# Kernel tuning notes

Measured on AMD Instinct MI355X. Metric: run time of the kernel, lower is better.

## Reference

```python
import jax, jax.numpy as jnp
import numpy as np

COST_CLASS, COST_BOX = 1.0, 5.0   # HungarianMatcher defaults
W_CLASS, W_BOX = 1.0, 5.0         # weight_dict
B, Q, M, NUM_CLASSES = 64, 900, 64, 4


def _hungarian(cost):
    """Jonker-Volgenant shortest augmenting path (same optimum as scipy's
    linear_sum_assignment). cost: [n, m] numpy, n <= m. Returns, for each
    row i, the assigned column index."""
    n, m = cost.shape
    u = np.zeros(n + 1, dtype=np.float64)
    v = np.zeros(m + 1, dtype=np.float64)
    p = np.zeros(m + 1, dtype=np.int64)    # p[j]: row matched to col j (1-based), 0=free
    way = np.zeros(m + 1, dtype=np.int64)
    cost = cost.astype(np.float64)
    for i in range(1, n + 1):
        p[0] = i
        j0 = 0
        minv = np.full(m + 1, np.inf)
        used = np.zeros(m + 1, dtype=bool)
        while True:
            used[j0] = True
            i0 = p[j0]
            cur = cost[i0 - 1, :] - u[i0] - v[1:]           # reduced costs, len m
            mask = ~used[1:]
            upd = mask & (cur < minv[1:])
            minv[1:][upd] = cur[upd]
            way[1:][upd] = j0
            cand = np.where(mask, minv[1:], np.inf)
            j1 = int(np.argmin(cand)) + 1
            delta = cand[j1 - 1]
            u[p[used]] += delta
            v[used] -= delta
            minv[1:][mask] -= delta
            j0 = j1
            if p[j0] == 0:
                break
        while j0 != 0:                                       # augment along path
            j1 = way[j0]
            p[j0] = p[j1]
            j0 = j1
    row_to_col = np.zeros(n, dtype=np.int64)
    for j in range(1, m + 1):
        if p[j] > 0:
            row_to_col[p[j] - 1] = j - 1
    return row_to_col


def _match(pred_boxes, pred_classes, gt_boxes, gt_labels, valid):
    """Host-side (no-grad) Hungarian matching, mirroring HungarianMatcher.
    Returns flat (batch_ids, pred_ids, gt_ids) numpy index arrays over all
    matched pairs; gt_ids index into the ORIGINAL [M] gt axis."""
    b_ids, p_ids, g_ids = [], [], []
    for b in range(pred_boxes.shape[0]):
        vpos = np.where(valid[b])[0]
        m = vpos.shape[0]
        if m == 0:
            continue
        logits = pred_classes[b]
        z = logits - logits.max(-1, keepdims=True)
        prob = np.exp(z)
        prob /= prob.sum(-1, keepdims=True)                  # softmax [Q, C]
        labels = gt_labels[b][vpos]
        cost_class = -prob[:, labels]                        # [Q, m]
        gb = gt_boxes[b][vpos]                               # [m, 6]
        cost_box = np.abs(pred_boxes[b][:, None, :] - gb[None, :, :]).sum(-1)  # L1 cdist [Q, m]
        cost = COST_CLASS * cost_class + COST_BOX * cost_box
        pred_idx = _hungarian(cost.T)                        # gt row -> pred col
        b_ids.append(np.full(m, b, dtype=np.int64))
        p_ids.append(pred_idx)
        g_ids.append(vpos.astype(np.int64))
    return (np.concatenate(b_ids), np.concatenate(p_ids), np.concatenate(g_ids))


def setup_inputs() -> dict:
    key = jax.random.key(0)
    k1, k2, k3, k4, k5 = jax.random.split(key, 5)
    return {
        "pred_boxes": jax.random.normal(k1, (B, Q, 6), dtype=jnp.float32),
        "pred_classes": jax.random.normal(k2, (B, Q, NUM_CLASSES), dtype=jnp.float32),
        "gt_boxes": jax.random.normal(k3, (B, M, 6), dtype=jnp.float32),
        "gt_labels": jax.random.randint(k4, (B, M), 0, NUM_CLASSES, dtype=jnp.int64),
        "gt_valid_mask": jax.random.bernoulli(k5, 0.8, (B, M)),
    }


def reference(pred_boxes, pred_classes, gt_boxes, gt_labels, gt_valid_mask):
    b_ids, p_ids, g_ids = _match(
        np.asarray(pred_boxes), np.asarray(pred_classes),
        np.asarray(gt_boxes), np.asarray(gt_labels), np.asarray(gt_valid_mask))
    n = b_ids.shape[0]
    labels = jnp.asarray(gt_labels)[b_ids, g_ids]            # [N]
    # class loss: mean cross-entropy over matched pairs
    logp = jax.nn.log_softmax(pred_classes[b_ids, p_ids], axis=-1)  # [N, C]
    class_loss = -jnp.mean(jnp.take_along_axis(logp, labels[:, None], axis=1))
    # box loss: elementwise-mean L1 over matched pairs
    box_loss = jnp.mean(jnp.abs(pred_boxes[b_ids, p_ids] - gt_boxes[b_ids, g_ids]))
    total_loss = W_CLASS * class_loss + W_BOX * box_loss
    return jnp.stack([class_loss, box_loss, total_loss])
```

## Files before the change

### kernel.cpp

```cpp
#include <hip/hip_runtime.h>
#include <cfloat>
#include <cmath>

#define NB 64
#define NQ 900
#define NM 64
#define NC 4
#define THREADS 256
#define NS 15

#define S_LIST(X) X(0) X(1) X(2) X(3) X(4) X(5) X(6) X(7) X(8) X(9) \
                  X(10) X(11) X(12) X(13) X(14)

__device__ __forceinline__ unsigned int uminu(unsigned int a, unsigned int b) {
    return a < b ? a : b;
}

__device__ __forceinline__ unsigned int wave_redmin_u32(unsigned int x) {
    int t;
    t = __builtin_amdgcn_update_dpp(-1, (int)x, 0x111, 0xF, 0xF, false);
    x = uminu(x, (unsigned)t);
    t = __builtin_amdgcn_update_dpp(-1, (int)x, 0x112, 0xF, 0xF, false);
    x = uminu(x, (unsigned)t);
    t = __builtin_amdgcn_update_dpp(-1, (int)x, 0x114, 0xF, 0xF, false);
    x = uminu(x, (unsigned)t);
    t = __builtin_amdgcn_update_dpp(-1, (int)x, 0x118, 0xF, 0xF, false);
    x = uminu(x, (unsigned)t);
    unsigned a = (unsigned)__builtin_amdgcn_readlane((int)x, 15);
    unsigned b = (unsigned)__builtin_amdgcn_readlane((int)x, 31);
    unsigned c = (unsigned)__builtin_amdgcn_readlane((int)x, 47);
    unsigned d = (unsigned)__builtin_amdgcn_readlane((int)x, 63);
    return uminu(uminu(a, b), uminu(c, d));
}

__device__ __forceinline__ void wave_argmin_f(float lmin, int lj,
                                              float& mv, int& mj) {
    unsigned u = __float_as_uint(lmin);
    unsigned key = (u & 0x80000000u) ? ~u : (u | 0x80000000u);
    unsigned mk = wave_redmin_u32(key);
    unsigned cand = (key == mk) ? (unsigned)lj : 0x7FFFFFFFu;
    mj = (int)wave_redmin_u32(cand);
    unsigned mu = (mk & 0x80000000u) ? (mk & 0x7FFFFFFFu) : ~mk;
    mv = __uint_as_float(mu);
}

__global__ __launch_bounds__(THREADS, 1) void match_kernel(
    const float* __restrict__ pred_boxes,
    const float* __restrict__ pred_classes,
    const float* __restrict__ gt_boxes,
    const unsigned int* __restrict__ labels_w,
    const unsigned int* __restrict__ mask_w,
    const unsigned char* __restrict__ mask_b,
    float* __restrict__ cls_part, float* __restrict__ box_part,
    int* __restrict__ cnt_part)
{
    __shared__ float4 pbx4[NQ];
    __shared__ float2 pbx2[NQ];
    __shared__ float  probT[NC][NQ];
    __shared__ int    pcol[NQ + 1];
    __shared__ int    claim[NQ];
    __shared__ float  upot[NM + 1];
    __shared__ int    tree_i[NM + 2];
    __shared__ float4 gb4[NM];
    __shared__ float2 gb2[NM];
    __shared__ int    lab[NM];
    __shared__ int    vpos_s[NM];
    __shared__ int    row2col[NM];
    __shared__ float  rowmin_s[NM];
    __shared__ int    rowarg_s[NM];
    __shared__ int    ua_s[NM];
    __shared__ int    nua_s;
    __shared__ int    m_sh;
    __shared__ int    f_lab_odd, f_m_not01, f_m_odd;
    __shared__ float  redc[4], redb[4];

    const int b = blockIdx.x;
    const int tid = threadIdx.x;
    const int lane = tid & 63;
    const int wv = tid >> 6;

    if (tid == 0) { f_lab_odd = 0; f_m_not01 = 0; f_m_odd = 0; }
    __syncthreads();

    for (int w = tid; w < 1024; w += THREADS) {
        unsigned int lw = labels_w[w];
        if ((w & 1) && lw != 0u) f_lab_odd = 1;
        unsigned int mw = mask_w[w];
        if (mw > 1u) f_m_not01 = 1;
        if ((w & 1) && mw != 0u) f_m_odd = 1;
    }
    for (int q = tid; q < NQ; q += THREADS) {
        const float4 lg = *reinterpret_cast<const float4*>(
            pred_classes + ((size_t)b * NQ + q) * NC);
        float mx = fmaxf(fmaxf(lg.x, lg.y), fmaxf(lg.z, lg.w));
        float e0 = expf(lg.x - mx), e1 = expf(lg.y - mx);
        float e2 = expf(lg.z - mx), e3 = expf(lg.w - mx);
        float inv = 1.0f / (e0 + e1 + e2 + e3);
        probT[0][q] = e0 * inv; probT[1][q] = e1 * inv;
        probT[2][q] = e2 * inv; probT[3][q] = e3 * inv;
        const float* bp = pred_boxes + ((size_t)b * NQ + q) * 6;
        float2 b0 = *reinterpret_cast<const float2*>(bp);
        float2 b1 = *reinterpret_cast<const float2*>(bp + 2);
        float2 b2 = *reinterpret_cast<const float2*>(bp + 4);
        pbx4[q] = make_float4(b0.x, b0.y, b1.x, b1.y);
        pbx2[q] = make_float2(b2.x, b2.y);
    }
    for (int j = tid; j <= NQ; j += THREADS) pcol[j] = 0;
    for (int j = tid; j < NQ; j += THREADS) claim[j] = 0x7FFFFFFF;
    for (int i2 = tid; i2 <= NM; i2 += THREADS) upot[i2] = 0.f;
    __syncthreads();

    const int lmode = f_lab_odd ? 0 : 1;
    const int mmode = f_m_not01 ? 2 : (f_m_odd ? 0 : 1);

    if (tid < 64) {
        int vv;
        if (mmode == 2)      vv = (mask_b[b * NM + lane] != 0);
        else if (mmode == 1) vv = (mask_w[(b * NM + lane) * 2] != 0u);
        else                 vv = (mask_w[b * NM + lane] != 0u);
        unsigned long long bal = __ballot(vv);
        if (vv) {
            int pos = (int)__popcll(bal & ((1ull << lane) - 1ull));
            vpos_s[pos] = lane;
        }
        if (lane == 0) m_sh = (int)__popcll(bal);
        __builtin_amdgcn_wave_barrier();
        int nw = (int)__popcll(bal);
        if (lane < nw) {
            int g = vpos_s[lane];
            lab[lane] = (int)(lmode ? labels_w[(size_t)(b * NM + g) * 2]
                                    : labels_w[b * NM + g]);
            const float* gp = gt_boxes + ((size_t)b * NM + g) * 6;
            gb4[lane] = make_float4(gp[0], gp[1], gp[2], gp[3]);
            gb2[lane] = make_float2(gp[4], gp[5]);
        }
    }
    __syncthreads();
    const int n = m_sh;

#define DECL_COL(s) float cb0_##s, cb1_##s, cb2_##s, cb3_##s, cb4_##s, cb5_##s;
    S_LIST(DECL_COL)
#define HOIST(s) { const int q = (s) * 64 + lane; \
        const int qc = (q < NQ) ? q : 0; \
        const float4 h4 = pbx4[qc]; const float2 h2 = pbx2[qc]; \
        cb0_##s = h4.x; cb1_##s = h4.y; cb2_##s = h4.z; cb3_##s = h4.w; \
        cb4_##s = h2.x; cb5_##s = h2.y; }
    S_LIST(HOIST)

    for (int k = wv; k < n; k += 4) {
        const float4 g4 = gb4[k];
        const float2 g2 = gb2[k];
        const float* prow = probT[lab[k]];
        float lmin = FLT_MAX; int lj = NQ + 2;
#define RSCAN(s) { const int q = (s) * 64 + lane; \
        const int qc = (q < NQ) ? q : 0; \
        float l1 = fabsf(cb0_##s - g4.x) + fabsf(cb1_##s - g4.y) \
                 + fabsf(cb2_##s - g4.z) + fabsf(cb3_##s - g4.w) \
                 + fabsf(cb4_##s - g2.x) + fabsf(cb5_##s - g2.y); \
        float c = 5.0f * l1 - prow[qc]; \
        if (q < NQ && c < lmin) { lmin = c; lj = q; } }
        S_LIST(RSCAN)
        float mv; int mj;
        wave_argmin_f(lmin, lj, mv, mj);
        if (lane == 0) { rowmin_s[k] = mv; rowarg_s[k] = mj; }
    }
    __syncthreads();

    if (tid < n) atomicMin(&claim[rowarg_s[tid]], tid);
    for (int k = tid; k < n; k += THREADS) upot[k + 1] = rowmin_s[k];
    if (tid == 0) upot[0] = 0.f;
    __syncthreads();
    if (tid < n) {
        int a = rowarg_s[tid];
        if (claim[a] == tid) pcol[a + 1] = tid + 1;
    }
    if (tid < 64) {
        int un = (lane < n) && (claim[rowarg_s[lane]] != lane);
        unsigned long long bal = __ballot(un);
        if (un) ua_s[(int)__popcll(bal & ((1ull << lane) - 1ull))] = lane;
        if (lane == 0) nua_s = (int)__popcll(bal);
    }
    __syncthreads();

    if (tid < 64) {
#define DECL_SAP(s) float minv_##s, vpot_##s; int way_##s;
        S_LIST(DECL_SAP)
#define INIT_VPOT(s) vpot_##s = 0.f;
        S_LIST(INIT_VPOT)
        const int nua = nua_s;

        for (int t = 0; t < nua; ++t) {
            const int i = ua_s[t] + 1;
#define INIT_MINV(s) { minv_##s = FLT_MAX; way_##s = 0; }
            S_LIST(INIT_MINV)
            unsigned int usedm = 0;
            if (lane == 0) pcol[0] = i;
            int j0 = 0, i0 = i, T = 0, bj = 0;
            while (true) {
                if (j0 > 0 && ((j0 - 1) & 63) == lane)
                    usedm |= 1u << ((j0 - 1) >> 6);
                if (lane == 0) tree_i[T] = i0;
                T++;
                __builtin_amdgcn_wave_barrier();
                const float base = upot[i0];
                const float4 g4 = gb4[i0 - 1];
                const float2 g2 = gb2[i0 - 1];
                const float* prow = probT[lab[i0 - 1]];
                float lmin = FLT_MAX; int lj = NQ + 2;
#define SSCAN(s) { const int q = (s) * 64 + lane; \
                const int qc = (q < NQ) ? q : 0; \
                float l1 = fabsf(cb0_##s - g4.x) + fabsf(cb1_##s - g4.y) \
                         + fabsf(cb2_##s - g4.z) + fabsf(cb3_##s - g4.w) \
                         + fabsf(cb4_##s - g2.x) + fabsf(cb5_##s - g2.y); \
                float cost = 5.0f * l1 - prow[qc]; \
                float cur = cost - base - vpot_##s; \
                if ((q < NQ) && !((usedm >> (s)) & 1u)) { \
                    if (cur < minv_##s) { minv_##s = cur; way_##s = j0; } \
                    if (minv_##s < lmin) { lmin = minv_##s; lj = q + 1; } } }
                S_LIST(SSCAN)
                float delta; int rbj;
                wave_argmin_f(lmin, lj, delta, rbj);
                bj = rbj;
                const int nr = pcol[bj];
                for (int tt = lane; tt < T; tt += 64)
                    upot[tree_i[tt]] += delta;
#define UPDATE(s) { if ((usedm >> (s)) & 1u) vpot_##s -= delta; \
                    else                     minv_##s -= delta; }
                S_LIST(UPDATE)
                __builtin_amdgcn_wave_barrier();
                if (nr == 0) break;
                j0 = bj; i0 = nr;
            }
            int jcur = bj;
            while (jcur != 0) {
                const int q = jcur - 1;
                const int sl = q >> 6, ln = q & 63;
                int wsel = 0;
#define WSEL(s) if (sl == (s)) wsel = way_##s;
                S_LIST(WSEL)
                const int jp = __builtin_amdgcn_readlane(wsel, ln);
                const int pv = pcol[jp];
                if (lane == 0) pcol[jcur] = pv;
                __builtin_amdgcn_wave_barrier();
                jcur = jp;
            }
        }
    }
    __syncthreads();

    for (int j = 1 + tid; j <= NQ; j += THREADS) {
        int r = pcol[j];
        if (r > 0) row2col[r - 1] = j - 1;
    }
    __syncthreads();
    float cs = 0.f, bs = 0.f;
    for (int k = tid; k < n; k += THREADS) {
        int q = row2col[k];
        int lb = lab[k];
        cs += -logf(probT[lb][q]);
        float4 p4 = pbx4[q]; float2 p2 = pbx2[q];
        float4 g4 = gb4[k];  float2 g2 = gb2[k];
        bs += fabsf(p4.x - g4.x) + fabsf(p4.y - g4.y) + fabsf(p4.z - g4.z)
            + fabsf(p4.w - g4.w) + fabsf(p2.x - g2.x) + fabsf(p2.y - g2.y);
    }
    for (int off = 32; off > 0; off >>= 1) {
        cs += __shfl_down(cs, off);
        bs += __shfl_down(bs, off);
    }
    {
        int wave = tid >> 6;
        if ((tid & 63) == 0) { redc[wave] = cs; redb[wave] = bs; }
    }
    __syncthreads();
    if (tid == 0) {
        cls_part[b] = redc[0] + redc[1] + redc[2] + redc[3];
        box_part[b] = redb[0] + redb[1] + redb[2] + redb[3];
        cnt_part[b] = n;
    }
}

__global__ void finalize_kernel(const float* __restrict__ cls_part,
                                const float* __restrict__ box_part,
                                const int* __restrict__ cnt_part,
                                float* __restrict__ out) {
    if (threadIdx.x == 0 && blockIdx.x == 0) {
        float c = 0.f, bx = 0.f;
        int nn = 0;
        for (int b = 0; b < NB; ++b) {
            c += cls_part[b]; bx += box_part[b]; nn += cnt_part[b];
        }
        float denom = (nn > 0) ? (float)nn : 1.0f;
        float cl = c / denom;
        float bl = bx / (6.0f * denom);
        out[0] = cl;
        out[1] = bl;
        out[2] = cl + 5.0f * bl;
    }
}

extern "C" void kernel_launch(void* const* d_in, const int* in_sizes, int n_in,
                              void* d_out, int out_size, void* d_ws, size_t ws_size,
                              hipStream_t stream) {
    const float* pred_boxes   = (const float*)d_in[0];
    const float* pred_classes = (const float*)d_in[1];
    const float* gt_boxes     = (const float*)d_in[2];
    const unsigned int*  labels_w = (const unsigned int*)d_in[3];
    const unsigned int*  mask_w   = (const unsigned int*)d_in[4];
    const unsigned char* mask_b   = (const unsigned char*)d_in[4];

    char* ws = (char*)d_ws;
    float* cls_part = (float*)(ws + 16);
    float* box_part = (float*)(ws + 16 + 4 * NB);
    int*   cnt_part = (int*)(ws + 16 + 8 * NB);
    float* out = (float*)d_out;

    match_kernel<<<NB, THREADS, 0, stream>>>(pred_boxes, pred_classes, gt_boxes,
                                             labels_w, mask_w, mask_b,
                                             cls_part, box_part, cnt_part);
    finalize_kernel<<<1, 64, 0, stream>>>(cls_part, box_part, cnt_part, out);
}
```

Before: 42.23 us.

## Keep row potentials and gt rows in registers, use contiguous per-lane columns

Moves the Hungarian row potentials, gt box coordinates and labels from shared memory into per-lane registers, broadcast with readlane during each augmenting-path step. The tree membership list is replaced by a per-lane flag. Columns are remapped so each of 60 lanes owns 15 contiguous queries, which removes bounds-clamping per slot. The argmin index is now picked with a ballot and readlane instead of a second wave reduction. Together these aim to cut LDS traffic and reduction latency in the serial, single-wave augmentation loop.

```diff
diff --git a/kernel.cpp b/kernel.cpp
--- a/kernel.cpp
+++ b/kernel.cpp
@@ -14,6 +14,11 @@
 
 __device__ __forceinline__ unsigned int uminu(unsigned int a, unsigned int b) {
     return a < b ? a : b;
+}
+
+__device__ __forceinline__ float readlane_f(float v, int l) {
+    return __uint_as_float(
+        (unsigned)__builtin_amdgcn_readlane(__float_as_int(v), l));
 }
 
 __device__ __forceinline__ unsigned int wave_redmin_u32(unsigned int x) {
@@ -38,8 +43,9 @@
     unsigned u = __float_as_uint(lmin);
     unsigned key = (u & 0x80000000u) ? ~u : (u | 0x80000000u);
     unsigned mk = wave_redmin_u32(key);
-    unsigned cand = (key == mk) ? (unsigned)lj : 0x7FFFFFFFu;
-    mj = (int)wave_redmin_u32(cand);
+    unsigned long long bal = __ballot(key == mk);
+    int fl = (int)__builtin_ctzll(bal);
+    mj = __builtin_amdgcn_readlane(lj, fl);
     unsigned mu = (mk & 0x80000000u) ? (mk & 0x7FFFFFFFu) : ~mk;
     mv = __uint_as_float(mu);
 }
@@ -59,8 +65,6 @@
     __shared__ float  probT[NC][NQ];
     __shared__ int    pcol[NQ + 1];
     __shared__ int    claim[NQ];
-    __shared__ float  upot[NM + 1];
-    __shared__ int    tree_i[NM + 2];
     __shared__ float4 gb4[NM];
     __shared__ float2 gb2[NM];
     __shared__ int    lab[NM];
@@ -107,7 +111,6 @@
     }
     for (int j = tid; j <= NQ; j += THREADS) pcol[j] = 0;
     for (int j = tid; j < NQ; j += THREADS) claim[j] = 0x7FFFFFFF;
-    for (int i2 = tid; i2 <= NM; i2 += THREADS) upot[i2] = 0.f;
     __syncthreads();
 
     const int lmode = f_lab_odd ? 0 : 1;
@@ -138,11 +141,12 @@
     __syncthreads();
     const int n = m_sh;
 
+    const bool lv = (lane < 60);
+    const int qb = lv ? lane * NS : 0;
 #define DECL_COL(s) float cb0_##s, cb1_##s, cb2_##s, cb3_##s, cb4_##s, cb5_##s;
     S_LIST(DECL_COL)
-#define HOIST(s) { const int q = (s) * 64 + lane; \
-        const int qc = (q < NQ) ? q : 0; \
-        const float4 h4 = pbx4[qc]; const float2 h2 = pbx2[qc]; \
+#define HOIST(s) { const float4 h4 = pbx4[qb + (s)]; \
+        const float2 h2 = pbx2[qb + (s)]; \
         cb0_##s = h4.x; cb1_##s = h4.y; cb2_##s = h4.z; cb3_##s = h4.w; \
         cb4_##s = h2.x; cb5_##s = h2.y; }
     S_LIST(HOIST)
@@ -152,13 +156,12 @@
         const float2 g2 = gb2[k];
         const float* prow = probT[lab[k]];
         float lmin = FLT_MAX; int lj = NQ + 2;
-#define RSCAN(s) { const int q = (s) * 64 + lane; \
-        const int qc = (q < NQ) ? q : 0; \
+#define RSCAN(s) { \
         float l1 = fabsf(cb0_##s - g4.x) + fabsf(cb1_##s - g4.y) \
                  + fabsf(cb2_##s - g4.z) + fabsf(cb3_##s - g4.w) \
                  + fabsf(cb4_##s - g2.x) + fabsf(cb5_##s - g2.y); \
-        float c = 5.0f * l1 - prow[qc]; \
-        if (q < NQ && c < lmin) { lmin = c; lj = q; } }
+        float c = 5.0f * l1 - prow[qb + (s)]; \
+        if (lv && c < lmin) { lmin = c; lj = qb + (s); } }
         S_LIST(RSCAN)
         float mv; int mj;
         wave_argmin_f(lmin, lj, mv, mj);
@@ -167,8 +170,6 @@
     __syncthreads();
 
     if (tid < n) atomicMin(&claim[rowarg_s[tid]], tid);
-    for (int k = tid; k < n; k += THREADS) upot[k + 1] = rowmin_s[k];
-    if (tid == 0) upot[0] = 0.f;
     __syncthreads();
     if (tid < n) {
         int a = rowarg_s[tid];
@@ -187,6 +188,14 @@
         S_LIST(DECL_SAP)
 #define INIT_VPOT(s) vpot_##s = 0.f;
         S_LIST(INIT_VPOT)
+        float ur = (lane < n) ? rowmin_s[lane] : 0.f;
+        float gr0 = 0.f, gr1 = 0.f, gr2 = 0.f, gr3 = 0.f, gr4 = 0.f, gr5 = 0.f;
+        int labr = 0;
+        if (lane < n) {
+            const float4 h4 = gb4[lane]; const float2 h2 = gb2[lane];
+            gr0 = h4.x; gr1 = h4.y; gr2 = h4.z; gr3 = h4.w;
+            gr4 = h2.x; gr5 = h2.y; labr = lab[lane];
+        }
         const int nua = nua_s;
 
         for (int t = 0; t < nua; ++t) {
@@ -194,36 +203,40 @@
 #define INIT_MINV(s) { minv_##s = FLT_MAX; way_##s = 0; }
             S_LIST(INIT_MINV)
             unsigned int usedm = 0;
+            int intree = 0;
             if (lane == 0) pcol[0] = i;
-            int j0 = 0, i0 = i, T = 0, bj = 0;
+            int j0 = 0, i0 = i, T_dummy = 0, bj = 0;
+            (void)T_dummy;
             while (true) {
-                if (j0 > 0 && ((j0 - 1) & 63) == lane)
-                    usedm |= 1u << ((j0 - 1) >> 6);
-                if (lane == 0) tree_i[T] = i0;
-                T++;
+                if (j0 > 0 && ((j0 - 1) / NS) == lane)
+                    usedm |= 1u << ((j0 - 1) % NS);
+                if (lane == i0 - 1) intree = 1;
                 __builtin_amdgcn_wave_barrier();
-                const float base = upot[i0];
-                const float4 g4 = gb4[i0 - 1];
-                const float2 g2 = gb2[i0 - 1];
-                const float* prow = probT[lab[i0 - 1]];
+                const float base = readlane_f(ur, i0 - 1);
+                const float g0 = readlane_f(gr0, i0 - 1);
+                const float g1 = readlane_f(gr1, i0 - 1);
+                const float g2 = readlane_f(gr2, i0 - 1);
+                const float g3 = readlane_f(gr3, i0 - 1);
+                const float g4 = readlane_f(gr4, i0 - 1);
+                const float g5 = readlane_f(gr5, i0 - 1);
+                const int lb = __builtin_amdgcn_readlane(labr, i0 - 1);
+                const float* prow = probT[lb];
                 float lmin = FLT_MAX; int lj = NQ + 2;
-#define SSCAN(s) { const int q = (s) * 64 + lane; \
-                const int qc = (q < NQ) ? q : 0; \
-                float l1 = fabsf(cb0_##s - g4.x) + fabsf(cb1_##s - g4.y) \
-                         + fabsf(cb2_##s - g4.z) + fabsf(cb3_##s - g4.w) \
-                         + fabsf(cb4_##s - g2.x) + fabsf(cb5_##s - g2.y); \
-                float cost = 5.0f * l1 - prow[qc]; \
+#define SSCAN(s) { \
+                float l1 = fabsf(cb0_##s - g0) + fabsf(cb1_##s - g1) \
+                         + fabsf(cb2_##s - g2) + fabsf(cb3_##s - g3) \
+                         + fabsf(cb4_##s - g4) + fabsf(cb5_##s - g5); \
+                float cost = 5.0f * l1 - prow[qb + (s)]; \
                 float cur = cost - base - vpot_##s; \
-                if ((q < NQ) && !((usedm >> (s)) & 1u)) { \
+                if (lv && !((usedm >> (s)) & 1u)) { \
                     if (cur < minv_##s) { minv_##s = cur; way_##s = j0; } \
-                    if (minv_##s < lmin) { lmin = minv_##s; lj = q + 1; } } }
+                    if (minv_##s < lmin) { lmin = minv_##s; lj = qb + (s) + 1; } } }
                 S_LIST(SSCAN)
                 float delta; int rbj;
                 wave_argmin_f(lmin, lj, delta, rbj);
                 bj = rbj;
                 const int nr = pcol[bj];
-                for (int tt = lane; tt < T; tt += 64)
-                    upot[tree_i[tt]] += delta;
+                if (intree) ur += delta;
 #define UPDATE(s) { if ((usedm >> (s)) & 1u) vpot_##s -= delta; \
                     else                     minv_##s -= delta; }
                 S_LIST(UPDATE)
@@ -234,11 +247,11 @@
             int jcur = bj;
             while (jcur != 0) {
                 const int q = jcur - 1;
-                const int sl = q >> 6, ln = q & 63;
+                const int li = q / NS, si = q % NS;
                 int wsel = 0;
-#define WSEL(s) if (sl == (s)) wsel = way_##s;
+#define WSEL(s) if (si == (s)) wsel = way_##s;
                 S_LIST(WSEL)
-                const int jp = __builtin_amdgcn_readlane(wsel, ln);
+                const int jp = __builtin_amdgcn_readlane(wsel, li);
                 const int pv = pcol[jp];
                 if (lane == 0) pcol[jcur] = pv;
                 __builtin_amdgcn_wave_barrier();
```

After: 42.16 us. No clear change (-0.2%).

## Spread Hungarian augmenting-path scan across all four waves of the block

Applied to the files above, without the earlier changes.

The shortest-augmenting-path phase previously ran on one wave, with each lane scanning 15 columns. Now all 256 threads each own 4 contiguous columns, with probabilities and boxes held in registers. The per-step argmin is reduced across waves through LDS with a block barrier, and the way array moves to LDS so thread 0 can augment serially. The initial row-min scan also uses all waves per row with a cross-wave merge, and the wave argmin uses ballot plus readlane instead of a second reduction. This cuts per-step scan work but adds two __syncthreads per step and a serial augmentation loop in thread 0.

```diff
diff --git a/kernel.cpp b/kernel.cpp
--- a/kernel.cpp
+++ b/kernel.cpp
@@ -7,10 +7,9 @@
 #define NM 64
 #define NC 4
 #define THREADS 256
-#define NS 15
-
-#define S_LIST(X) X(0) X(1) X(2) X(3) X(4) X(5) X(6) X(7) X(8) X(9) \
-                  X(10) X(11) X(12) X(13) X(14)
+#define NCT 225
+
+#define S4_LIST(X) X(0) X(1) X(2) X(3)
 
 __device__ __forceinline__ unsigned int uminu(unsigned int a, unsigned int b) {
     return a < b ? a : b;
@@ -38,8 +37,9 @@
     unsigned u = __float_as_uint(lmin);
     unsigned key = (u & 0x80000000u) ? ~u : (u | 0x80000000u);
     unsigned mk = wave_redmin_u32(key);
-    unsigned cand = (key == mk) ? (unsigned)lj : 0x7FFFFFFFu;
-    mj = (int)wave_redmin_u32(cand);
+    unsigned long long bal = __ballot(key == mk);
+    int fl = (int)__builtin_ctzll(bal);
+    mj = __builtin_amdgcn_readlane(lj, fl);
     unsigned mu = (mk & 0x80000000u) ? (mk & 0x7FFFFFFFu) : ~mk;
     mv = __uint_as_float(mu);
 }
@@ -59,8 +59,8 @@
     __shared__ float  probT[NC][NQ];
     __shared__ int    pcol[NQ + 1];
     __shared__ int    claim[NQ];
+    __shared__ int    way_lds[NQ + 1];
     __shared__ float  upot[NM + 1];
-    __shared__ int    tree_i[NM + 2];
     __shared__ float4 gb4[NM];
     __shared__ float2 gb2[NM];
     __shared__ int    lab[NM];
@@ -68,10 +68,14 @@
     __shared__ int    row2col[NM];
     __shared__ float  rowmin_s[NM];
     __shared__ int    rowarg_s[NM];
+    __shared__ float  rpart_v[4][NM];
+    __shared__ int    rpart_j[4][NM];
     __shared__ int    ua_s[NM];
     __shared__ int    nua_s;
     __shared__ int    m_sh;
     __shared__ int    f_lab_odd, f_m_not01, f_m_odd;
+    __shared__ __align__(16) float redv[4];
+    __shared__ __align__(16) int   redj[4];
     __shared__ float  redc[4], redb[4];
 
     const int b = blockIdx.x;
@@ -105,9 +109,8 @@
         pbx4[q] = make_float4(b0.x, b0.y, b1.x, b1.y);
         pbx2[q] = make_float2(b2.x, b2.y);
     }
-    for (int j = tid; j <= NQ; j += THREADS) pcol[j] = 0;
+    for (int j = tid; j <= NQ; j += THREADS) { pcol[j] = 0; way_lds[j] = 0; }
     for (int j = tid; j < NQ; j += THREADS) claim[j] = 0x7FFFFFFF;
-    for (int i2 = tid; i2 <= NM; i2 += THREADS) upot[i2] = 0.f;
     __syncthreads();
 
     const int lmode = f_lab_odd ? 0 : 1;
@@ -138,31 +141,57 @@
     __syncthreads();
     const int n = m_sh;
 
+    const bool lv = (tid < NCT);
+    const int qb = lv ? (tid << 2) : 0;
 #define DECL_COL(s) float cb0_##s, cb1_##s, cb2_##s, cb3_##s, cb4_##s, cb5_##s;
-    S_LIST(DECL_COL)
-#define HOIST(s) { const int q = (s) * 64 + lane; \
-        const int qc = (q < NQ) ? q : 0; \
-        const float4 h4 = pbx4[qc]; const float2 h2 = pbx2[qc]; \
+    S4_LIST(DECL_COL)
+    float cq0_0, cq0_1, cq0_2, cq0_3;
+    float cq1_0, cq1_1, cq1_2, cq1_3;
+    float cq2_0, cq2_1, cq2_2, cq2_3;
+    float cq3_0, cq3_1, cq3_2, cq3_3;
+#define HOIST(s) { const float4 h4 = pbx4[qb + (s)]; \
+        const float2 h2 = pbx2[qb + (s)]; \
         cb0_##s = h4.x; cb1_##s = h4.y; cb2_##s = h4.z; cb3_##s = h4.w; \
         cb4_##s = h2.x; cb5_##s = h2.y; }
-    S_LIST(HOIST)
-
-    for (int k = wv; k < n; k += 4) {
+    S4_LIST(HOIST)
+    {
+        const float4 p0 = *reinterpret_cast<const float4*>(&probT[0][qb]);
+        const float4 p1 = *reinterpret_cast<const float4*>(&probT[1][qb]);
+        const float4 p2 = *reinterpret_cast<const float4*>(&probT[2][qb]);
+        const float4 p3 = *reinterpret_cast<const float4*>(&probT[3][qb]);
+        cq0_0 = p0.x; cq0_1 = p0.y; cq0_2 = p0.z; cq0_3 = p0.w;
+        cq1_0 = p1.x; cq1_1 = p1.y; cq1_2 = p1.z; cq1_3 = p1.w;
+        cq2_0 = p2.x; cq2_1 = p2.y; cq2_2 = p2.z; cq2_3 = p2.w;
+        cq3_0 = p3.x; cq3_1 = p3.y; cq3_2 = p3.z; cq3_3 = p3.w;
+    }
+
+    for (int k = 0; k < n; ++k) {
         const float4 g4 = gb4[k];
         const float2 g2 = gb2[k];
-        const float* prow = probT[lab[k]];
+        const int lb = lab[k];
         float lmin = FLT_MAX; int lj = NQ + 2;
-#define RSCAN(s) { const int q = (s) * 64 + lane; \
-        const int qc = (q < NQ) ? q : 0; \
+#define RSCAN(s) { \
         float l1 = fabsf(cb0_##s - g4.x) + fabsf(cb1_##s - g4.y) \
                  + fabsf(cb2_##s - g4.z) + fabsf(cb3_##s - g4.w) \
                  + fabsf(cb4_##s - g2.x) + fabsf(cb5_##s - g2.y); \
-        float c = 5.0f * l1 - prow[qc]; \
-        if (q < NQ && c < lmin) { lmin = c; lj = q; } }
-        S_LIST(RSCAN)
+        float pr = (lb == 0) ? cq0_##s : ((lb == 1) ? cq1_##s \
+                 : ((lb == 2) ? cq2_##s : cq3_##s)); \
+        float c = 5.0f * l1 - pr; \
+        if (lv && c < lmin) { lmin = c; lj = qb + (s); } }
+        S4_LIST(RSCAN)
         float mv; int mj;
         wave_argmin_f(lmin, lj, mv, mj);
-        if (lane == 0) { rowmin_s[k] = mv; rowarg_s[k] = mj; }
+        if (lane == 0) { rpart_v[wv][k] = mv; rpart_j[wv][k] = mj; }
+    }
+    __syncthreads();
+    if (tid < n) {
+        float bv = rpart_v[0][tid]; int bj = rpart_j[0][tid];
+        #pragma unroll
+        for (int w = 1; w < 4; ++w) {
+            float vw = rpart_v[w][tid]; int jw = rpart_j[w][tid];
+            if (vw < bv || (vw == bv && jw < bj)) { bv = vw; bj = jw; }
+        }
+        rowmin_s[tid] = bv; rowarg_s[tid] = bj;
     }
     __syncthreads();
 
@@ -182,67 +211,71 @@
     }
     __syncthreads();
 
-    if (tid < 64) {
-#define DECL_SAP(s) float minv_##s, vpot_##s; int way_##s;
-        S_LIST(DECL_SAP)
-#define INIT_VPOT(s) vpot_##s = 0.f;
-        S_LIST(INIT_VPOT)
+    {
+        float minv_0, minv_1, minv_2, minv_3;
+        float vpot_0 = 0.f, vpot_1 = 0.f, vpot_2 = 0.f, vpot_3 = 0.f;
         const int nua = nua_s;
 
         for (int t = 0; t < nua; ++t) {
             const int i = ua_s[t] + 1;
-#define INIT_MINV(s) { minv_##s = FLT_MAX; way_##s = 0; }
-            S_LIST(INIT_MINV)
+            minv_0 = FLT_MAX; minv_1 = FLT_MAX;
+            minv_2 = FLT_MAX; minv_3 = FLT_MAX;
             unsigned int usedm = 0;
-            if (lane == 0) pcol[0] = i;
-            int j0 = 0, i0 = i, T = 0, bj = 0;
+            int intree = 0;
+            if (tid == 0) pcol[0] = i;
+            int j0 = 0, i0 = i, bj = 0;
+            __syncthreads();
             while (true) {
-                if (j0 > 0 && ((j0 - 1) & 63) == lane)
-                    usedm |= 1u << ((j0 - 1) >> 6);
-                if (lane == 0) tree_i[T] = i0;
-                T++;
-                __builtin_amdgcn_wave_barrier();
+                if (j0 > 0 && ((j0 - 1) >> 2) == tid)
+                    usedm |= 1u << ((j0 - 1) & 3);
+                if (tid == i0 - 1) intree = 1;
                 const float base = upot[i0];
                 const float4 g4 = gb4[i0 - 1];
                 const float2 g2 = gb2[i0 - 1];
-                const float* prow = probT[lab[i0 - 1]];
+                const int lb = lab[i0 - 1];
                 float lmin = FLT_MAX; int lj = NQ + 2;
-#define SSCAN(s) { const int q = (s) * 64 + lane; \
-                const int qc = (q < NQ) ? q : 0; \
+#define SSCAN(s) { \
                 float l1 = fabsf(cb0_##s - g4.x) + fabsf(cb1_##s - g4.y) \
                          + fabsf(cb2_##s - g4.z) + fabsf(cb3_##s - g4.w) \
                          + fabsf(cb4_##s - g2.x) + fabsf(cb5_##s - g2.y); \
-                float cost = 5.0f * l1 - prow[qc]; \
+                float pr = (lb == 0) ? cq0_##s : ((lb == 1) ? cq1_##s \
+                         : ((lb == 2) ? cq2_##s : cq3_##s)); \
+                float cost = 5.0f * l1 - pr; \
                 float cur = cost - base - vpot_##s; \
-                if ((q < NQ) && !((usedm >> (s)) & 1u)) { \
-                    if (cur < minv_##s) { minv_##s = cur; way_##s = j0; } \
-                    if (minv_##s < lmin) { lmin = minv_##s; lj = q + 1; } } }
-                S_LIST(SSCAN)
-                float delta; int rbj;
-                wave_argmin_f(lmin, lj, delta, rbj);
-                bj = rbj;
+                if (lv && !((usedm >> (s)) & 1u)) { \
+                    if (cur < minv_##s) { minv_##s = cur; \
+                                          way_lds[qb + (s) + 1] = j0; } \
+                    if (minv_##s < lmin) { lmin = minv_##s; \
+                                           lj = qb + (s) + 1; } } }
+                S4_LIST(SSCAN)
+                float pv; int pj;
+                wave_argmin_f(lmin, lj, pv, pj);
+                if (lane == 0) { redv[wv] = pv; redj[wv] = pj; }
+                __syncthreads();
+                const float4 rv4 = *reinterpret_cast<const float4*>(redv);
+                const int4   rj4 = *reinterpret_cast<const int4*>(redj);
+                float dv = rv4.x; int dj = rj4.x;
+                if (rv4.y < dv || (rv4.y == dv && rj4.y < dj)) { dv = rv4.y; dj = rj4.y; }
+                if (rv4.z < dv || (rv4.z == dv && rj4.z < dj)) { dv = rv4.z; dj = rj4.z; }
+                if (rv4.w < dv || (rv4.w == dv && rj4.w < dj)) { dv = rv4.w; dj = rj4.w; }
+                const float delta = dv;
+                bj = dj;
                 const int nr = pcol[bj];
-                for (int tt = lane; tt < T; tt += 64)
-                    upot[tree_i[tt]] += delta;
 #define UPDATE(s) { if ((usedm >> (s)) & 1u) vpot_##s -= delta; \
                     else                     minv_##s -= delta; }
-                S_LIST(UPDATE)
-                __builtin_amdgcn_wave_barrier();
+                S4_LIST(UPDATE)
+                if (intree) upot[tid + 1] += delta;
+                __syncthreads();
                 if (nr == 0) break;
                 j0 = bj; i0 = nr;
             }
-            int jcur = bj;
-            while (jcur != 0) {
-                const int q = jcur - 1;
-                const int sl = q >> 6, ln = q & 63;
-                int wsel = 0;
-#define WSEL(s) if (sl == (s)) wsel = way_##s;
-                S_LIST(WSEL)
-                const int jp = __builtin_amdgcn_readlane(wsel, ln);
-                const int pv = pcol[jp];
-                if (lane == 0) pcol[jcur] = pv;
-                __builtin_amdgcn_wave_barrier();
-                jcur = jp;
+            if (tid == 0) {
+                int jcur = bj;
+                while (jcur != 0) {
+                    int jp = way_lds[jcur];
+                    pcol[jcur] = pcol[jp];
+                    jcur = jp;
+                }
             }
         }
     }
```

Measured after the change: 40.46 us. 4.2% less time.
